# Kernel optimization log

Measured on AMD Instinct MI355X. Metric: run time of the kernel, lower is better.

## Reference

```python
import jax, jax.numpy as jnp
import numpy as np
from jax import lax


def _lstm_dir(x_gates, Whh, bhh, reverse):
    # x_gates: (B,T,4H) = x @ Wih.T + bih, precomputed for all timesteps
    B, T, G = x_gates.shape
    H = G // 4

    def step(carry, xg):
        h, c = carry
        g = xg + h @ Whh.T + bhh
        i, f, gg, o = jnp.split(g, 4, axis=-1)  # PyTorch gate order i,f,g,o
        c = jax.nn.sigmoid(f) * c + jax.nn.sigmoid(i) * jnp.tanh(gg)
        h = jax.nn.sigmoid(o) * jnp.tanh(c)
        return (h, c), h

    xs = jnp.swapaxes(x_gates, 0, 1)  # (T,B,4H)
    if reverse:
        xs = xs[::-1]
    init = (jnp.zeros((B, H), x_gates.dtype), jnp.zeros((B, H), x_gates.dtype))
    _, hs = lax.scan(step, init, xs)
    if reverse:
        hs = hs[::-1]
    return jnp.swapaxes(hs, 0, 1)  # (B,T,H)


def _forward(embeddings, mask,
             enc_Wih_f, enc_Whh_f, enc_bih_f, enc_bhh_f,
             enc_Wih_b, enc_Whh_b, enc_bih_b, enc_bhh_b,
             attn_W, attn_b, tag_embed,
             dec_Wih, dec_Whh, dec_bih, dec_bhh,
             Wout, bout):
    B, T, D = embeddings.shape
    maskf = mask.astype(embeddings.dtype)

    # --- bidirectional encoder ---
    xg_f = jnp.einsum('btd,gd->btg', embeddings, enc_Wih_f) + enc_bih_f
    xg_b = jnp.einsum('btd,gd->btg', embeddings, enc_Wih_b) + enc_bih_b
    out_f = _lstm_dir(xg_f, enc_Whh_f, enc_bhh_f, False)
    out_b = _lstm_dir(xg_b, enc_Whh_b, enc_bhh_b, True)
    output = jnp.concatenate([out_f, out_b], axis=-1) * maskf[:, :, None]  # (B,T,2H)

    lengths = mask.sum(axis=1) - 1
    last_output = output[jnp.arange(B), lengths]  # (B,2H)

    def attend(v):
        # AllenNLP BilinearAttention: softmax(v @ W @ M^T + b), then * mask
        sc = jnp.einsum('bd,de,bte->bt', v, attn_W, output) + attn_b
        return jax.nn.softmax(sc, axis=-1) * maskf

    context0 = jnp.einsum('bt,btd->bd', attend(last_output), output)  # (B,2H)

    Hd = output.shape[-1]          # decoder hidden = 2H
    E = tag_embed.shape[1]         # tag embedding dim (== hidden_size)
    h0 = jnp.zeros((B, Hd), embeddings.dtype)
    c0 = jnp.zeros((B, Hd), embeddings.dtype)

    def step(carry, xt):
        h, c, context, last_tag = carry
        aligned, i = xt
        emb = jnp.where(i == 0,
                        jnp.zeros((B, E), embeddings.dtype),
                        tag_embed[last_tag])
        dec_input = jnp.concatenate([emb, context, aligned], axis=-1)  # (B, E+4H)
        g = dec_input @ dec_Wih.T + dec_bih + h @ dec_Whh.T + dec_bhh
        ii, f, gg, o = jnp.split(g, 4, axis=-1)
        c = jax.nn.sigmoid(f) * c + jax.nn.sigmoid(ii) * jnp.tanh(gg)
        h = jax.nn.sigmoid(o) * jnp.tanh(c)
        concated = jnp.concatenate([h, context], axis=-1)  # (B,4H)
        score = concated @ Wout.T + bout                   # (B,V)
        new_context = jnp.einsum('bt,btd->bd', attend(h), output)
        last_tag = jnp.argmax(score, axis=-1).astype(jnp.int32)
        return (h, c, new_context, last_tag), score

    xs = (jnp.swapaxes(output, 0, 1), jnp.arange(T))
    init = (h0, c0, context0, jnp.zeros((B,), jnp.int32))
    _, scores = lax.scan(step, init, xs)  # (T,B,V)
    return jnp.swapaxes(scores, 0, 1)     # (B,T,V) slot logits


def setup_inputs() -> dict:
    key = jax.random.key(0)
    B, T, D, H, E, V = 32, 64, 512, 512, 512, 2048
    H2 = 2 * H
    dec_in = E + 2 * H2  # tag_emb + context(2H) + aligned(2H)
    ks = jax.random.split(key, 20)
    s = 0.02
    f32 = jnp.float32
    return {
        'embeddings': jax.random.normal(ks[0], (B, T, D), f32),
        'mask': jnp.ones((B, T), jnp.int32),
        'enc_Wih_f': jax.random.normal(ks[1], (4 * H, D), f32) * s,
        'enc_Whh_f': jax.random.normal(ks[2], (4 * H, H), f32) * s,
        'enc_bih_f': jax.random.normal(ks[3], (4 * H,), f32) * s,
        'enc_bhh_f': jax.random.normal(ks[4], (4 * H,), f32) * s,
        'enc_Wih_b': jax.random.normal(ks[5], (4 * H, D), f32) * s,
        'enc_Whh_b': jax.random.normal(ks[6], (4 * H, H), f32) * s,
        'enc_bih_b': jax.random.normal(ks[7], (4 * H,), f32) * s,
        'enc_bhh_b': jax.random.normal(ks[8], (4 * H,), f32) * s,
        'attn_W': jax.random.normal(ks[9], (H2, H2), f32) * s,
        'attn_b': jax.random.normal(ks[10], (), f32) * s,
        'tag_embed': jax.random.normal(ks[11], (V, E), f32) * s,
        'dec_Wih': jax.random.normal(ks[12], (4 * H2, dec_in), f32) * s,
        'dec_Whh': jax.random.normal(ks[13], (4 * H2, H2), f32) * s,
        'dec_bih': jax.random.normal(ks[14], (4 * H2,), f32) * s,
        'dec_bhh': jax.random.normal(ks[15], (4 * H2,), f32) * s,
        'Wout': jax.random.normal(ks[16], (V, 2 * H2), f32) * s,
        'bout': jax.random.normal(ks[17], (V,), f32) * s,
    }


def reference(embeddings, mask,
              enc_Wih_f, enc_Whh_f, enc_bih_f, enc_bhh_f,
              enc_Wih_b, enc_Whh_b, enc_bih_b, enc_bhh_b,
              attn_W, attn_b, tag_embed,
              dec_Wih, dec_Whh, dec_bih, dec_bhh,
              Wout, bout):
    return _forward(embeddings, mask,
                    enc_Wih_f, enc_Whh_f, enc_bih_f, enc_bhh_f,
                    enc_Wih_b, enc_Whh_b, enc_bih_b, enc_bhh_b,
                    attn_W, attn_b, tag_embed,
                    dec_Wih, dec_Whh, dec_bih, dec_bhh,
                    Wout, bout)
```

## Files before the change

kernel.cpp:

```cpp
#include <hip/hip_runtime.h>

#define B   32
#define T   64
#define D   512
#define H   512
#define H2  1024
#define G4  4096
#define V   2048
#define DEC_IN 2560

__device__ __forceinline__ float sigm(float x) { return 1.f / (1.f + expf(-x)); }

__device__ __forceinline__ unsigned fenc(float f) {
  unsigned u = __float_as_uint(f);
  return (u & 0x80000000u) ? ~u : (u | 0x80000000u);
}

__device__ __forceinline__ void st_wt(float* p, float v) {
  __hip_atomic_store(p, v, __ATOMIC_RELAXED, __HIP_MEMORY_SCOPE_AGENT);
}

__device__ __forceinline__ void pbar(unsigned* slots, unsigned* flags, int myid, int nblk) {
  __syncthreads();
  if (threadIdx.x == 0)
    __hip_atomic_store(slots + myid, 1u, __ATOMIC_RELAXED, __HIP_MEMORY_SCOPE_AGENT);
  if (myid == 0) {
    for (int s = threadIdx.x; s < nblk; s += 256) {
      while (!__hip_atomic_load(slots + s, __ATOMIC_RELAXED, __HIP_MEMORY_SCOPE_AGENT))
        __builtin_amdgcn_s_sleep(1);
    }
    __syncthreads();
    if (threadIdx.x < 16)
      __hip_atomic_store(flags + threadIdx.x*16, 1u, __ATOMIC_RELAXED, __HIP_MEMORY_SCOPE_AGENT);
  }
  if (threadIdx.x == 0) {
    unsigned* f = flags + (myid & 15)*16;
    while (!__hip_atomic_load(f, __ATOMIC_RELAXED, __HIP_MEMORY_SCOPE_AGENT))
      __builtin_amdgcn_s_sleep(1);
    (void)__hip_atomic_load(f, __ATOMIC_ACQUIRE, __HIP_MEMORY_SCOPE_AGENT);
  }
  __syncthreads();
}

__global__ __launch_bounds__(256) void gemm_nt(
    const float* __restrict__ A, int lda,
    const float* __restrict__ W, int ldw,
    float* __restrict__ C, int ldc,
    const float* __restrict__ bias0, const float* __restrict__ bias1,
    int K)
{
  __shared__ float As[8][132];
  __shared__ float Bs[8][132];
  const int tid = threadIdx.x;
  const int nb = blockIdx.x * 128;
  const int mb = blockIdx.y * 128;
  const int tx = tid & 15;
  const int ty = tid >> 4;
  float acc[8][8] = {};

  const int am = tid >> 1, ak = (tid & 1) * 4;
  const float* aptr = A + (size_t)(mb + am) * lda + ak;
  const float* bptr = W + (size_t)(nb + am) * ldw + ak;

  for (int k0 = 0; k0 < K; k0 += 8) {
    float4 av = *(const float4*)(aptr + k0);
    float4 bv = *(const float4*)(bptr + k0);
    As[ak+0][am] = av.x; As[ak+1][am] = av.y; As[ak+2][am] = av.z; As[ak+3][am] = av.w;
    Bs[ak+0][am] = bv.x; Bs[ak+1][am] = bv.y; Bs[ak+2][am] = bv.z; Bs[ak+3][am] = bv.w;
    __syncthreads();
    #pragma unroll
    for (int k = 0; k < 8; ++k) {
      float4 a0 = *(const float4*)&As[k][ty*8];
      float4 a1 = *(const float4*)&As[k][ty*8+4];
      float4 b0 = *(const float4*)&Bs[k][tx*8];
      float4 b1 = *(const float4*)&Bs[k][tx*8+4];
      float avv[8] = {a0.x,a0.y,a0.z,a0.w,a1.x,a1.y,a1.z,a1.w};
      float bvv[8] = {b0.x,b0.y,b0.z,b0.w,b1.x,b1.y,b1.z,b1.w};
      #pragma unroll
      for (int i = 0; i < 8; ++i)
        #pragma unroll
        for (int j = 0; j < 8; ++j)
          acc[i][j] += avv[i]*bvv[j];
    }
    __syncthreads();
  }
  float b8[8];
  #pragma unroll
  for (int j = 0; j < 8; ++j) {
    float bvv = 0.f;
    if (bias0) bvv += bias0[nb + tx*8 + j];
    if (bias1) bvv += bias1[nb + tx*8 + j];
    b8[j] = bvv;
  }
  #pragma unroll
  for (int i = 0; i < 8; ++i) {
    float4 o0, o1;
    o0.x = acc[i][0]+b8[0]; o0.y = acc[i][1]+b8[1]; o0.z = acc[i][2]+b8[2]; o0.w = acc[i][3]+b8[3];
    o1.x = acc[i][4]+b8[4]; o1.y = acc[i][5]+b8[5]; o1.z = acc[i][6]+b8[6]; o1.w = acc[i][7]+b8[7];
    size_t idx = (size_t)(mb + ty*8 + i) * ldc + nb + tx*8;
    *(float4*)&C[idx]     = o0;
    *(float4*)&C[idx + 4] = o1;
  }
}

__device__ void attend_slice(int ab, int aslice, const float* __restrict__ hvec,
                             float* __restrict__ ctxdst,
                             const float* __restrict__ outbuf, const float* __restrict__ projo,
                             const int* __restrict__ mask, float* scratch, int tid)
{
  float* scp = scratch;
  float* scv = scratch + 256;
  float* p2  = scratch + 320;
  const int tq = tid >> 2, dq = tid & 3;
  const float4* hv = (const float4*)(hvec + dq*256);
  const float4* pv = (const float4*)(projo + (size_t)(ab*T + tq)*H2 + dq*256);
  float p = 0.f;
  #pragma unroll 8
  for (int k4 = 0; k4 < 64; ++k4) {
    float4 a = hv[k4], q = pv[k4];
    p += a.x*q.x + a.y*q.y + a.z*q.z + a.w*q.w;
  }
  scp[tid] = p;
  __syncthreads();
  if (tid < 64) {
    float v = scp[tid*4] + scp[tid*4+1] + scp[tid*4+2] + scp[tid*4+3];
    float mx = v;
    #pragma unroll
    for (int d = 32; d; d >>= 1) mx = fmaxf(mx, __shfl_xor(mx, d, 64));
    float e = expf(v - mx);
    float sm = e;
    #pragma unroll
    for (int d = 32; d; d >>= 1) sm += __shfl_xor(sm, d, 64);
    scv[tid] = e * (1.f / sm) * (float)mask[ab*T + tid];
  }
  __syncthreads();
  {
    const int dl = tid & 127, th = tid >> 7;
    const int dg = aslice*128 + dl;
    float acc = 0.f;
    #pragma unroll 8
    for (int q = 0; q < 32; ++q) {
      int tt = th*32 + q;
      acc += scv[tt] * outbuf[(size_t)(ab*T + tt)*H2 + dg];
    }
    if (th == 1) p2[dl] = acc;
    __syncthreads();
    if (th == 0) st_wt(&ctxdst[dg*32 + ab], acc + p2[dl]);
  }
}

__global__ __launch_bounds__(256, 1) void encoder_persistent(
    const float* __restrict__ xg_f, const float* __restrict__ xg_b,
    const float* __restrict__ Whh_f, const float* __restrict__ Whh_b,
    const int* __restrict__ mask,
    float* __restrict__ hencT,
    float* __restrict__ outbuf,
    unsigned* __restrict__ eslots, unsigned* __restrict__ eflags)
{
  __shared__ float S_lds[9216];
  __shared__ float pacc[2048];
  __shared__ float g_lds[512];
  const int blk = blockIdx.x, tid = threadIdx.x;
  const int lane = tid & 63, wv = tid >> 6;
  const int dir = blk >> 7, nd = blk & 127;
  const int hibase = nd * 4;
  const int jj = tid & 7, kk = tid >> 3;
  const int kkl = lane >> 3;
  const float* xg  = dir ? xg_b : xg_f;
  const float* Whh = dir ? Whh_b : Whh_f;
  float* hbase = hencT + dir * 32768;
  float* Sw = S_lds + wv*2304;

  float wge[2][16];
  #pragma unroll
  for (int p = 0; p < 2; ++p) {
    int jl = jj*2 + p;
    int j = (jl>>2)*512 + hibase + (jl&3);
    #pragma unroll
    for (int sc = 0; sc < 4; ++sc)
      #pragma unroll
      for (int i = 0; i < 4; ++i)
        wge[p][sc*4+i] = Whh[(size_t)j*512 + sc*128 + i*32 + kk];
  }
  float c_reg = 0.f;
  const int lr = lane >> 1, halfc = (lane & 1) * 16;
  const int grow = (lr >> 3)*32 + 8*wv + (lr & 7);

  for (int tt = 0; tt < 64; ++tt) {
    const int t = dir ? (63 - tt) : tt;
    const float* hc = hbase + (tt & 1) * 16384;
    float* hn = hbase + ((tt + 1) & 1) * 16384;

    float a0[32], a1[32];
    #pragma unroll
    for (int q = 0; q < 32; ++q) { a0[q] = 0.f; a1[q] = 0.f; }

    float4 r0, r1, r2, r3;
    {
      const float4* p = (const float4*)(hc + grow*32 + halfc);
      r0 = p[0]; r1 = p[1]; r2 = p[2]; r3 = p[3];
      float* d = Sw + lr*36 + halfc;
      *(float4*)d = r0; *(float4*)(d+4) = r1; *(float4*)(d+8) = r2; *(float4*)(d+12) = r3;
    }
    #pragma unroll
    for (int sc = 0; sc < 4; ++sc) {
      if (sc < 3) {
        const float4* p = (const float4*)(hc + ((sc+1)*128 + grow)*32 + halfc);
        r0 = p[0]; r1 = p[1]; r2 = p[2]; r3 = p[3];
      }
      const float* Sb = Sw + (sc & 1)*1152;
      #pragma unroll
      for (int i = 0; i < 4; ++i) {
        const float* sp = Sb + (i*8 + kkl)*36;
        float w0 = wge[0][sc*4+i], w1 = wge[1][sc*4+i];
        #pragma unroll
        for (int q = 0; q < 8; ++q) {
          float4 s4 = *(const float4*)(sp + q*4);
          a0[q*4+0] += w0*s4.x; a0[q*4+1] += w0*s4.y; a0[q*4+2] += w0*s4.z; a0[q*4+3] += w0*s4.w;
          a1[q*4+0] += w1*s4.x; a1[q*4+1] += w1*s4.y; a1[q*4+2] += w1*s4.z; a1[q*4+3] += w1*s4.w;
        }
      }
      if (sc < 3) {
        float* d = Sw + ((sc+1) & 1)*1152 + lr*36 + halfc;
        *(float4*)d = r0; *(float4*)(d+4) = r1; *(float4*)(d+8) = r2; *(float4*)(d+12) = r3;
      }
    }
    #pragma unroll
    for (int dd = 8; dd <= 32; dd <<= 1) {
      #pragma unroll
      for (int q = 0; q < 32; ++q) {
        a0[q] += __shfl_down(a0[q], dd, 64);
        a1[q] += __shfl_down(a1[q], dd, 64);
      }
    }
    if (lane < 8) {
      float* pw = &pacc[wv*512 + lane*64];
      #pragma unroll
      for (int q = 0; q < 32; ++q) { pw[q] = a0[q]; pw[32+q] = a1[q]; }
    }
    __syncthreads();
    #pragma unroll
    for (int r = 0; r < 2; ++r) {
      int o = tid + r*256;
      int jl = o >> 5, b = o & 31;
      int off = (jl>>1)*64 + (jl&1)*32 + b;
      float v = pacc[off] + pacc[512+off] + pacc[1024+off] + pacc[1536+off];
      v += xg[(size_t)(b*T + t)*2048 + (jl>>2)*512 + hibase + (jl&3)];
      g_lds[jl*32 + b] = v;
    }
    __syncthreads();
    if (tid < 128) {
      int hil = tid >> 5, b = tid & 31;
      float gi = g_lds[(0*4+hil)*32 + b];
      float gf = g_lds[(1*4+hil)*32 + b];
      float gg = g_lds[(2*4+hil)*32 + b];
      float go = g_lds[(3*4+hil)*32 + b];
      c_reg = sigm(gf)*c_reg + sigm(gi)*tanhf(gg);
      float h = sigm(go)*tanhf(c_reg);
      int hi = hibase + hil;
      st_wt(&hn[hi*32 + b], h);
      st_wt(&outbuf[(size_t)(b*T + t)*H2 + dir*512 + hi], h * (float)mask[b*T + t]);
    }
    pbar(eslots + (dir*64 + tt)*128, eflags + (dir*64 + tt)*256, nd, 128);
  }
}

#define GROW1(lr) (8*wv + ((lr) < 8 ? (lr) : 24 + (lr)))
#define GROW2(lr) (16*wv + (lr))
#define SLDG(qq, s) { int krr = (s)*64 + GROW1(lrow); \
  const float* bs = (krr < 1024) ? (hTc + krr*32) : (ctxc + (krr-1024)*32); \
  qq##a = *(const float4*)(bs + scol2); qq##b = *(const float4*)(bs + scol2 + 4); }
#define SLDS(qq, s) { int krr = (s)*64 + GROW2(lrow); \
  const float* bs = (krr < 1024) ? (hTn + krr*32) : (ctxc + (krr-1024)*32); \
  qq##a = *(const float4*)(bs + scol2); qq##b = *(const float4*)(bs + scol2 + 4); }
#define STW(qq, BUF) { float* d = Sw + (BUF)*576 + lrow*36 + scol2; \
  *(float4*)d = qq##a; *(float4*)(d+4) = qq##b; }
#define COMPG(sl, BUF) { const float* Sb = Sw + (BUF)*576; \
  _Pragma("unroll") for (int i = 0; i < 2; ++i) { \
    float w0 = Wg[jl0*2052 + (sl)*64 + i*32 + kkg]; \
    float w1 = Wg[jl1*2052 + (sl)*64 + i*32 + kkg]; \
    const float* sp = Sb + (i*8 + kkl)*36; \
    _Pragma("unroll") for (int q = 0; q < 8; ++q) { \
      float4 s4 = *(const float4*)(sp + q*4); \
      a0[q*4+0] += w0*s4.x; a0[q*4+1] += w0*s4.y; a0[q*4+2] += w0*s4.z; a0[q*4+3] += w0*s4.w; \
      a1[q*4+0] += w1*s4.x; a1[q*4+1] += w1*s4.y; a1[q*4+2] += w1*s4.z; a1[q*4+3] += w1*s4.w; } } }
#define COMPS(sl, BUF) { const float* sp = Sw + (BUF)*576 + lrow*36; \
  float w0 = ws0[sl], w1 = ws1[sl]; \
  _Pragma("unroll") for (int q = 0; q < 8; ++q) { \
    float4 s4 = *(const float4*)(sp + q*4); \
    a0[q*4+0] += w0*s4.x; a0[q*4+1] += w0*s4.y; a0[q*4+2] += w0*s4.z; a0[q*4+3] += w0*s4.w; \
    a1[q*4+0] += w1*s4.x; a1[q*4+1] += w1*s4.y; a1[q*4+2] += w1*s4.z; a1[q*4+3] += w1*s4.w; } }

__global__ __launch_bounds__(256, 1) void decoder_persistent(
    const float* __restrict__ basep, const float* __restrict__ tagp,
    const float* __restrict__ dWhh,  const float* __restrict__ dWih,
    const float* __restrict__ Wout,  const float* __restrict__ bout,
    const float* __restrict__ projo, const float* __restrict__ outbuf,
    const int* __restrict__ mask,
    float* __restrict__ hT,
    float* __restrict__ ctxT,
    float* __restrict__ hrow,
    unsigned long long* __restrict__ argslot,
    unsigned* __restrict__ dslots, unsigned* __restrict__ dflags,
    float* __restrict__ out)
{
  extern __shared__ float dyn[];
  float* Wg    = dyn;
  float* S2    = dyn + 32832;
  float* pacc  = dyn + 37440;
  float* g_lds = dyn + 39488;

  const int blk = blockIdx.x, tid = threadIdx.x;
  const int lane = tid & 63, wv = tid >> 6;
  const int hibase = blk * 4;
  const int jj = lane & 7, kkl = lane >> 3;
  const int kkg = 8*wv + kkl;
  const int jl0 = jj*2, jl1 = jj*2 + 1;
  const int vv = tid & 3, kq = tid >> 2;
  const int vbase = blk * 8;
  const int lrow = lane >> 2, scol2 = (lane & 3) * 8;
  const int ab = blk & 31, aslice = blk >> 5;
  float* Sw = S2 + wv*1152;

  for (int jl = 0; jl < 16; ++jl) {
    int j = (jl>>2)*1024 + hibase + (jl&3);
    #pragma unroll
    for (int r = 0; r < 2; ++r) {
      int c = tid*4 + r*1024;
      float4 w;
      if (c < 1024) w = *(const float4*)(dWhh + (size_t)j*1024 + c);
      else          w = *(const float4*)(dWih + (size_t)j*2560 + 512 + (c - 1024));
      *(float4*)&Wg[jl*2052 + c] = w;
    }
  }
  float ws0[32], ws1[32];
  {
    int v0 = vbase + vv*2;
    #pragma unroll
    for (int s2 = 0; s2 < 32; ++s2) {
      ws0[s2] = Wout[(size_t)(v0+0)*2048 + s2*64 + kq];
      ws1[s2] = Wout[(size_t)(v0+1)*2048 + s2*64 + kq];
    }
  }

  float c_reg = 0.f;
  int bslot = 0;

  {
    int len = -1;
    for (int i = 0; i < T; ++i) len += mask[ab*T + i];
    attend_slice(ab, aslice, outbuf + (size_t)(ab*T + len)*H2, ctxT,
                 outbuf, projo, mask, pacc, tid);
  }
  pbar(dslots + (bslot)*256, dflags + (bslot)*256, blk, 256); bslot++;

  for (int t = 0; t < T; ++t) {
    const int cur = t & 1, nxt = cur ^ 1;
    const float* hTc  = hT + cur*32768;
    float*       hTn  = hT + nxt*32768;
    const float* ctxc = ctxT + cur*32768;
    float*       ctxn = ctxT + nxt*32768;

    const int b_own = tid & 31;
    const int jlA = tid >> 5, jlB = jlA + 8;
    const int jA = (jlA>>2)*1024 + hibase + (jlA&3);
    const int jB = (jlB>>2)*1024 + hibase + (jlB&3);
    float extA = basep[(size_t)(b_own*T + t)*G4 + jA];
    float extB = basep[(size_t)(b_own*T + t)*G4 + jB];
    if (t > 0) {
      unsigned long long sl64 = __hip_atomic_load(&argslot[((t+2)%3)*32 + b_own],
                                                  __ATOMIC_RELAXED, __HIP_MEMORY_SCOPE_AGENT);
      unsigned tg = ~(unsigned)sl64;
      extA += tagp[(size_t)tg*G4 + jA];
      extB += tagp[(size_t)tg*G4 + jB];
    }

    float a0[32], a1[32];
    #pragma unroll
    for (int q = 0; q < 32; ++q) { a0[q] = 0.f; a1[q] = 0.f; }
    {
      float4 q0a,q0b,q1a,q1b,q2a,q2b,q3a,q3b;
      SLDG(q0, 0) SLDG(q1, 1) SLDG(q2, 2) SLDG(q3, 3)
      STW(q0, 0)
      for (int g = 0; g < 8; ++g) {
        const int sl = g*4;
        if (sl+4 < 32) SLDG(q0, sl+4)
        COMPG(sl, 0)
        STW(q1, 1)
        if (sl+5 < 32) SLDG(q1, sl+5)
        COMPG(sl+1, 1)
        STW(q2, 0)
        if (sl+6 < 32) SLDG(q2, sl+6)
        COMPG(sl+2, 0)
        STW(q3, 1)
        if (sl+7 < 32) SLDG(q3, sl+7)
        COMPG(sl+3, 1)
        if (sl+4 < 32) STW(q0, 0)
      }
    }
    #pragma unroll
    for (int dd = 8; dd <= 32; dd <<= 1) {
      #pragma unroll
      for (int q = 0; q < 32; ++q) {
        a0[q] += __shfl_down(a0[q], dd, 64);
        a1[q] += __shfl_down(a1[q], dd, 64);
      }
    }
    if (lane < 8) {
      float* pw = &pacc[wv*512 + lane*64];
      #pragma unroll
      for (int q = 0; q < 32; ++q) { pw[q] = a0[q]; pw[32+q] = a1[q]; }
    }
    __syncthreads();
    #pragma unroll
    for (int r = 0; r < 2; ++r) {
      int o = tid + r*256;
      int jl = o >> 5, b = o & 31;
      int off = (jl>>1)*64 + (jl&1)*32 + b;
      float vsum = pacc[off] + pacc[512+off] + pacc[1024+off] + pacc[1536+off];
      vsum += (r == 0) ? extA : extB;
      g_lds[jl*32 + b] = vsum;
    }
    __syncthreads();
    if (tid < 128) {
      int hil = tid >> 5, b = tid & 31;
      float gi = g_lds[(0*4+hil)*32 + b];
      float gf = g_lds[(1*4+hil)*32 + b];
      float gg = g_lds[(2*4+hil)*32 + b];
      float go = g_lds[(3*4+hil)*32 + b];
      c_reg = sigm(gf)*c_reg + sigm(gi)*tanhf(gg);
      float h = sigm(go)*tanhf(c_reg);
      int hi = hibase + hil;
      st_wt(&hTn[hi*32 + b], h);
      st_wt(&hrow[b*1024 + hi], h);
    }
    pbar(dslots + (bslot)*256, dflags + (bslot)*256, blk, 256); bslot++;

    #pragma unroll
    for (int q = 0; q < 32; ++q) { a0[q] = 0.f; a1[q] = 0.f; }
    {
      float4 q0a,q0b,q1a,q1b,q2a,q2b,q3a,q3b;
      SLDS(q0, 0) SLDS(q1, 1) SLDS(q2, 2) SLDS(q3, 3)
      STW(q0, 0)
      #pragma unroll
      for (int g = 0; g < 8; ++g) {
        const int sl = g*4;
        if (sl+4 < 32) SLDS(q0, sl+4)
        COMPS(sl, 0)
        STW(q1, 1)
        if (sl+5 < 32) SLDS(q1, sl+5)
        COMPS(sl+1, 1)
        STW(q2, 0)
        if (sl+6 < 32) SLDS(q2, sl+6)
        COMPS(sl+2, 0)
        STW(q3, 1)
        if (sl+7 < 32) SLDS(q3, sl+7)
        COMPS(sl+3, 1)
        if (sl+4 < 32) STW(q0, 0)
      }
    }
    #pragma unroll
    for (int dd = 4; dd <= 32; dd <<= 1) {
      #pragma unroll
      for (int q = 0; q < 32; ++q) {
        a0[q] += __shfl_down(a0[q], dd, 64);
        a1[q] += __shfl_down(a1[q], dd, 64);
      }
    }
    if (lane < 4) {
      float* pw = &pacc[wv*256 + lane*64];
      #pragma unroll
      for (int q = 0; q < 32; ++q) { pw[q] = a0[q]; pw[32+q] = a1[q]; }
    }
    __syncthreads();
    {
      int vl = tid & 7, b = tid >> 3;
      int off = (vl>>1)*64 + (vl&1)*32 + b;
      float s = pacc[off] + pacc[256+off] + pacc[512+off] + pacc[768+off];
      s += bout[vbase + vl];
      st_wt(&out[(size_t)(b*T + t)*V + vbase + vl], s);
      g_lds[vl*32 + b] = s;
    }
    __syncthreads();
    if (tid < 32) {
      int b = tid;
      float best = g_lds[b]; int bi = 0;
      #pragma unroll
      for (int vl = 1; vl < 8; ++vl) {
        float s = g_lds[vl*32 + b];
        if (s > best) { best = s; bi = vl; }
      }
      unsigned long long e = ((unsigned long long)fenc(best) << 32)
                           | (unsigned long long)(unsigned)(~(unsigned)(vbase + bi));
      atomicMax(&argslot[(t%3)*32 + b], e);
    } else if (blk == 0 && tid >= 32 && tid < 64) {
      __hip_atomic_store(&argslot[((t+1)%3)*32 + (tid - 32)], 0ull,
                         __ATOMIC_RELAXED, __HIP_MEMORY_SCOPE_AGENT);
    }
    if (t < 63) {
      __syncthreads();
      attend_slice(ab, aslice, hrow + ab*1024, ctxn, outbuf, projo, mask, pacc, tid);
    }
    pbar(dslots + (bslot)*256, dflags + (bslot)*256, blk, 256); bslot++;
  }
}

extern "C" void kernel_launch(void* const* d_in, const int* in_sizes, int n_in,
                              void* d_out, int out_size, void* d_ws, size_t ws_size,
                              hipStream_t stream)
{
  (void)in_sizes; (void)n_in; (void)out_size; (void)ws_size;
  const float* emb    = (const float*)d_in[0];
  const int*   mask   = (const int*)d_in[1];
  const float* Wih_f  = (const float*)d_in[2];
  const float* Whh_f  = (const float*)d_in[3];
  const float* bih_f  = (const float*)d_in[4];
  const float* bhh_f  = (const float*)d_in[5];
  const float* Wih_b  = (const float*)d_in[6];
  const float* Whh_b  = (const float*)d_in[7];
  const float* bih_b  = (const float*)d_in[8];
  const float* bhh_b  = (const float*)d_in[9];
  const float* attnW  = (const float*)d_in[10];
  const float* tagemb = (const float*)d_in[12];
  const float* dWih   = (const float*)d_in[13];
  const float* dWhh   = (const float*)d_in[14];
  const float* dbih   = (const float*)d_in[15];
  const float* dbhh   = (const float*)d_in[16];
  const float* Wout   = (const float*)d_in[17];
  const float* bout   = (const float*)d_in[18];
  float* out = (float*)d_out;

  float* ws = (float*)d_ws;
  float* xg_f   = ws + 0;
  float* xg_b   = ws + 4194304;
  float* outbuf = ws + 8388608;
  float* projo  = ws + 10485760;
  float* basep  = ws + 12582912;
  float* tagp   = ws + 20971520;
  float* hT     = ws + 29360128;
  float* ctxT   = ws + 29425664;
  float* hrow   = ws + 29491200;
  float* hencT  = ws + 29523968;
  unsigned long long* argslot = (unsigned long long*)(ws + 29589504);
  unsigned* dslots = (unsigned*)(ws + 29589696);
  unsigned* dflags = (unsigned*)(ws + 29622720);
  unsigned* eslots = (unsigned*)(ws + 29655744);
  unsigned* eflags = (unsigned*)(ws + 29672128);

  (void)hipFuncSetAttribute((const void*)decoder_persistent,
                            hipFuncAttributeMaxDynamicSharedMemorySize, 160000);

  hipMemsetAsync((void*)(ws + 29360128), 0, (size_t)(29704896 - 29360128) * sizeof(float), stream);

  gemm_nt<<<dim3(16, 16), 256, 0, stream>>>(emb, 512, Wih_f, 512, xg_f, 2048, bih_f, bhh_f, 512);
  gemm_nt<<<dim3(16, 16), 256, 0, stream>>>(emb, 512, Wih_b, 512, xg_b, 2048, bih_b, bhh_b, 512);
  gemm_nt<<<dim3(32, 16), 256, 0, stream>>>(tagemb, 512, dWih, DEC_IN, tagp, G4, nullptr, nullptr, 512);
  encoder_persistent<<<256, 256, 0, stream>>>(xg_f, xg_b, Whh_f, Whh_b, mask, hencT, outbuf, eslots, eflags);
  gemm_nt<<<dim3(8, 16), 256, 0, stream>>>(outbuf, H2, attnW, H2, projo, H2, nullptr, nullptr, H2);
  gemm_nt<<<dim3(32, 16), 256, 0, stream>>>(outbuf, H2, dWih + 1536, DEC_IN, basep, G4, dbih, dbhh, H2);
  decoder_persistent<<<256, 256, 160000, stream>>>(basep, tagp, dWhh, dWih, Wout, bout,
                                                   projo, outbuf, mask, hT, ctxT, hrow,
                                                   argslot, dslots, dflags, out);
}
```

Measured before the change: 4.729 ms.

## Use per-timestep decoder state buffers and drop acquire load in grid barrier

The decoder's double-buffered hidden, context and row buffers become one buffer per timestep, carved from the xg workspace, which is dead once the encoder finishes. Because every address is written only once, stale cache lines can never be read. That allows a barrier variant that skips the final acquire load, and with it the cache invalidation on each of the three grid barriers per step. The risk is correctness: without acquire ordering, reads could in principle see stale data if the relaxed stores and loads do not bypass the non-coherent caches as assumed.

Result: faster. 4.548 ms (-3.8%).

```diff
diff --git a/kernel.cpp b/kernel.cpp
--- a/kernel.cpp
+++ b/kernel.cpp
@@ -38,6 +38,27 @@
     while (!__hip_atomic_load(f, __ATOMIC_RELAXED, __HIP_MEMORY_SCOPE_AGENT))
       __builtin_amdgcn_s_sleep(1);
     (void)__hip_atomic_load(f, __ATOMIC_ACQUIRE, __HIP_MEMORY_SCOPE_AGENT);
+  }
+  __syncthreads();
+}
+
+__device__ __forceinline__ void pbar_na(unsigned* slots, unsigned* flags, int myid, int nblk) {
+  __syncthreads();
+  if (threadIdx.x == 0)
+    __hip_atomic_store(slots + myid, 1u, __ATOMIC_RELAXED, __HIP_MEMORY_SCOPE_AGENT);
+  if (myid == 0) {
+    for (int s = threadIdx.x; s < nblk; s += 256) {
+      while (!__hip_atomic_load(slots + s, __ATOMIC_RELAXED, __HIP_MEMORY_SCOPE_AGENT))
+        __builtin_amdgcn_s_sleep(1);
+    }
+    __syncthreads();
+    if (threadIdx.x < 16)
+      __hip_atomic_store(flags + threadIdx.x*16, 1u, __ATOMIC_RELAXED, __HIP_MEMORY_SCOPE_AGENT);
+  }
+  if (threadIdx.x == 0) {
+    unsigned* f = flags + (myid & 15)*16;
+    while (!__hip_atomic_load(f, __ATOMIC_RELAXED, __HIP_MEMORY_SCOPE_AGENT))
+      __builtin_amdgcn_s_sleep(1);
   }
   __syncthreads();
 }
@@ -297,9 +318,10 @@
     const float* __restrict__ Wout,  const float* __restrict__ bout,
     const float* __restrict__ projo, const float* __restrict__ outbuf,
     const int* __restrict__ mask,
-    float* __restrict__ hT,
-    float* __restrict__ ctxT,
-    float* __restrict__ hrow,
+    float* __restrict__ hbufs,
+    float* __restrict__ cbufs,
+    float* __restrict__ rbufs,
+    const float* __restrict__ zeroh,
     unsigned long long* __restrict__ argslot,
     unsigned* __restrict__ dslots, unsigned* __restrict__ dflags,
     float* __restrict__ out)
@@ -349,17 +371,17 @@
   {
     int len = -1;
     for (int i = 0; i < T; ++i) len += mask[ab*T + i];
-    attend_slice(ab, aslice, outbuf + (size_t)(ab*T + len)*H2, ctxT,
+    attend_slice(ab, aslice, outbuf + (size_t)(ab*T + len)*H2, cbufs,
                  outbuf, projo, mask, pacc, tid);
   }
-  pbar(dslots + (bslot)*256, dflags + (bslot)*256, blk, 256); bslot++;
+  pbar_na(dslots + (bslot)*256, dflags + (bslot)*256, blk, 256); bslot++;
 
   for (int t = 0; t < T; ++t) {
-    const int cur = t & 1, nxt = cur ^ 1;
-    const float* hTc  = hT + cur*32768;
-    float*       hTn  = hT + nxt*32768;
-    const float* ctxc = ctxT + cur*32768;
-    float*       ctxn = ctxT + nxt*32768;
+    const float* hTc  = (t == 0) ? zeroh : (hbufs + (size_t)(t-1)*32768);
+    float*       hTn  = hbufs + (size_t)t*32768;
+    const float* ctxc = cbufs + (size_t)t*32768;
+    float*       ctxn = cbufs + (size_t)(t+1)*32768;
+    float*       hrw  = rbufs + (size_t)t*32768;
 
     const int b_own = tid & 31;
     const int jlA = tid >> 5, jlB = jlA + 8;
@@ -432,9 +454,9 @@
       float h = sigm(go)*tanhf(c_reg);
       int hi = hibase + hil;
       st_wt(&hTn[hi*32 + b], h);
-      st_wt(&hrow[b*1024 + hi], h);
-    }
-    pbar(dslots + (bslot)*256, dflags + (bslot)*256, blk, 256); bslot++;
+      st_wt(&hrw[b*1024 + hi], h);
+    }
+    pbar_na(dslots + (bslot)*256, dflags + (bslot)*256, blk, 256); bslot++;
 
     #pragma unroll
     for (int q = 0; q < 32; ++q) { a0[q] = 0.f; a1[q] = 0.f; }
@@ -499,9 +521,9 @@
     }
     if (t < 63) {
       __syncthreads();
-      attend_slice(ab, aslice, hrow + ab*1024, ctxn, outbuf, projo, mask, pacc, tid);
-    }
-    pbar(dslots + (bslot)*256, dflags + (bslot)*256, blk, 256); bslot++;
+      attend_slice(ab, aslice, hrw + ab*1024, ctxn, outbuf, projo, mask, pacc, tid);
+    }
+    pbar_na(dslots + (bslot)*256, dflags + (bslot)*256, blk, 256); bslot++;
   }
 }
 
@@ -533,13 +555,14 @@
   float* ws = (float*)d_ws;
   float* xg_f   = ws + 0;
   float* xg_b   = ws + 4194304;
+  float* hbufs  = ws + 0;
+  float* cbufs  = ws + 2097152;
+  float* rbufs  = ws + 4227072;
   float* outbuf = ws + 8388608;
   float* projo  = ws + 10485760;
   float* basep  = ws + 12582912;
   float* tagp   = ws + 20971520;
-  float* hT     = ws + 29360128;
-  float* ctxT   = ws + 29425664;
-  float* hrow   = ws + 29491200;
+  float* zeroh  = ws + 29360128;
   float* hencT  = ws + 29523968;
   unsigned long long* argslot = (unsigned long long*)(ws + 29589504);
   unsigned* dslots = (unsigned*)(ws + 29589696);
@@ -559,6 +582,6 @@
   gemm_nt<<<dim3(8, 16), 256, 0, stream>>>(outbuf, H2, attnW, H2, projo, H2, nullptr, nullptr, H2);
   gemm_nt<<<dim3(32, 16), 256, 0, stream>>>(outbuf, H2, dWih + 1536, DEC_IN, basep, G4, dbih, dbhh, H2);
   decoder_persistent<<<256, 256, 160000, stream>>>(basep, tagp, dWhh, dWih, Wout, bout,
-                                                   projo, outbuf, mask, hT, ctxT, hrow,
+                                                   projo, outbuf, mask, hbufs, cbufs, rbufs, zeroh,
                                                    argslot, dslots, dflags, out);
 }
```
